# Kernel optimization log

Measured on AMD Instinct MI355X. Metric: run time of the kernel, lower is better.

The kernel has to match this reference:

```python
import jax, jax.numpy as jnp
import numpy as np

H = 4096          # hidden_size
NIN = 17          # RFSIZE*RFSIZE + ADDINPUT + NBACTIONS = 9+4+4
NA = 4            # NBACTIONS


def setup_inputs() -> dict:
    key = jax.random.key(0)
    ks = jax.random.split(key, 12)
    return {
        "x": jax.random.normal(ks[0], (1, NIN), jnp.float32),
        "hidden": 0.1 * jax.random.normal(ks[1], (1, H), jnp.float32),
        "hebb": 0.01 * jax.random.normal(ks[2], (H, H), jnp.float32),
        "i2h_w": 0.1 * jax.random.normal(ks[3], (H, NIN), jnp.float32),
        "i2h_b": 0.1 * jax.random.normal(ks[4], (H,), jnp.float32),
        "w": 0.01 * jax.random.uniform(ks[5], (H, H), jnp.float32),
        "alpha": 0.01 * jax.random.uniform(ks[6], (H, H), jnp.float32),
        "eta": 0.01 * jnp.ones((1,), jnp.float32),
        "h2o_w": 0.1 * jax.random.normal(ks[7], (NA, H), jnp.float32),
        "h2o_b": 0.1 * jax.random.normal(ks[8], (NA,), jnp.float32),
        "h2v_w": 0.1 * jax.random.normal(ks[9], (1, H), jnp.float32),
        "h2v_b": 0.1 * jax.random.normal(ks[10], (1,), jnp.float32),
    }


def reference(x, hidden, hebb, i2h_w, i2h_b, w, alpha, eta, h2o_w, h2o_b, h2v_w, h2v_b):
    # plastic RNN step: h = tanh(i2h(x) + hidden @ (w + alpha*hebb))
    h = jnp.tanh(x @ i2h_w.T + i2h_b + hidden @ (w + alpha * hebb))  # [1,H]
    # Hebbian trace update: (1-eta)*hebb + eta * outer(hidden, h)
    hebb_new = (1.0 - eta) * hebb + eta * (hidden[0][:, None] * h[0][None, :])  # [H,H]
    activout = jax.nn.softmax(h @ h2o_w.T + h2o_b, axis=-1)  # [1,NA]
    valueout = h @ h2v_w.T + h2v_b                           # [1,1]
    return activout, valueout, h, hebb_new
```

## Files before the change

kernel.cpp:

```cpp
#include <hip/hip_runtime.h>

#define HDIM 4096
#define NIN 17
#define NA 4

using f4 = __attribute__((ext_vector_type(4))) float;

constexpr int TB = 256;
constexpr int CPT = 4;
constexpr int BXC = HDIM / (TB * CPT);
constexpr int NCHUNK = 1024;
constexpr int RPC = HDIM / NCHUNK;
constexpr size_t NELEM = (size_t)HDIM * HDIM;

__global__ void k_matvec(const float* __restrict__ w, const float* __restrict__ alpha,
                         const float* __restrict__ hebb, const float* __restrict__ hidden,
                         float* __restrict__ partial, float* __restrict__ acc5) {
    if (blockIdx.x == 0 && blockIdx.y == 0 && threadIdx.x < 8) acc5[threadIdx.x] = 0.f;
    const int col0 = (blockIdx.x * TB + threadIdx.x) * CPT;
    const int row0 = blockIdx.y * RPC;
    const size_t base = (size_t)row0 * HDIM + col0;

    f4 wv[RPC], av[RPC], bv[RPC];
#pragma unroll
    for (int r = 0; r < RPC; ++r) {
        const size_t off = base + (size_t)r * HDIM;
        wv[r] = __builtin_nontemporal_load((const f4*)(w + off));
        av[r] = __builtin_nontemporal_load((const f4*)(alpha + off));
        bv[r] = *(const f4*)(hebb + off);
    }
    f4 acc = {0.f, 0.f, 0.f, 0.f};
#pragma unroll
    for (int r = 0; r < RPC; ++r) {
        const float hv = hidden[row0 + r];
        acc += hv * (wv[r] + av[r] * bv[r]);
    }
    *(f4*)(partial + (size_t)blockIdx.y * HDIM + col0) = acc;
}

constexpr int HC = 32;
constexpr int HGRP = TB / HC;
constexpr int HCPG = NCHUNK / HGRP;

__global__ void k_hact(const float* __restrict__ partial, const float* __restrict__ x,
                       const float* __restrict__ i2h_w, const float* __restrict__ i2h_b,
                       const float* __restrict__ h2o_w, const float* __restrict__ h2v_w,
                       float* __restrict__ h_f, float* __restrict__ h_out,
                       float* __restrict__ acc5) {
    const int tid = threadIdx.x;
    const int lane = tid & (HC - 1);
    const int grp = tid >> 5;
    const int col = blockIdx.x * HC + lane;

    float s = 0.f;
    const float* p = partial + (size_t)(grp * HCPG) * HDIM + col;
#pragma unroll 16
    for (int c = 0; c < HCPG; ++c) s += p[(size_t)c * HDIM];

    __shared__ float red[TB];
    red[tid] = s;
    __syncthreads();
    for (int st = TB / 2; st >= HC; st >>= 1) {
        if (tid < st) red[tid] += red[tid + st];
        __syncthreads();
    }
    if (tid < HC) {
        float z = red[tid] + i2h_b[col];
#pragma unroll
        for (int k = 0; k < NIN; ++k) z += x[k] * i2h_w[col * NIN + k];
        const float h = tanhf(z);
        h_f[col] = h;
        h_out[col] = h;
        float d[NA + 1];
#pragma unroll
        for (int a = 0; a < NA; ++a) d[a] = h * h2o_w[(size_t)a * HDIM + col];
        d[NA] = h * h2v_w[col];
#pragma unroll
        for (int a = 0; a <= NA; ++a) {
            float v = d[a];
#pragma unroll
            for (int sft = 16; sft > 0; sft >>= 1) v += __shfl_down(v, sft, 32);
            if (lane == 0) atomicAdd(acc5 + a, v);
        }
    }
}

__global__ void k_hebb(const float* __restrict__ hebb, const float* __restrict__ hidden,
                       const float* __restrict__ h_f, const float* __restrict__ eta,
                       float* __restrict__ hebb_out) {
    const size_t t = (size_t)blockIdx.x * TB + threadIdx.x;
    const size_t s = 4 * t + 3;
    const float e = eta[0];
    const float om = 1.f - e;

    if (t == 0) {
        const float hv0 = e * hidden[0];
        hebb_out[0] = om * hebb[0] + hv0 * h_f[0];
        hebb_out[1] = om * hebb[1] + hv0 * h_f[1];
        hebb_out[2] = om * hebb[2] + hv0 * h_f[2];
    }

    if (s + 3 < NELEM) {
        const float b0 = hebb[s];
        const f4 bv = *(const f4*)(hebb + s + 1);
        const float b[4] = {b0, bv.x, bv.y, bv.z};
        f4 v;
#pragma unroll
        for (int k = 0; k < 4; ++k) {
            const size_t m = s + (size_t)k;
            const int i = (int)(m >> 12);
            const int jj = (int)(m & (HDIM - 1));
            v[k] = om * b[k] + e * hidden[i] * h_f[jj];
        }
        __builtin_nontemporal_store(v, (f4*)(hebb_out + s));
    } else {
        for (size_t m = s; m < NELEM; ++m) {
            const int i = (int)(m >> 12);
            const int jj = (int)(m & (HDIM - 1));
            hebb_out[m] = om * hebb[m] + e * hidden[i] * h_f[jj];
        }
    }
}

__global__ __launch_bounds__(64)
void k_finish(const float* __restrict__ acc5,
              const float* __restrict__ h2o_b, const float* __restrict__ h2v_b,
              float* __restrict__ out) {
    if (threadIdx.x == 0) {
        float o[NA];
        float mx = -1e30f;
#pragma unroll
        for (int a = 0; a < NA; ++a) { o[a] = acc5[a] + h2o_b[a]; mx = fmaxf(mx, o[a]); }
        float se = 0.f;
#pragma unroll
        for (int a = 0; a < NA; ++a) { o[a] = __expf(o[a] - mx); se += o[a]; }
#pragma unroll
        for (int a = 0; a < NA; ++a) out[a] = o[a] / se;
        out[NA] = acc5[NA] + h2v_b[0];
    }
}

extern "C" void kernel_launch(void* const* d_in, const int* in_sizes, int n_in,
                              void* d_out, int out_size, void* d_ws, size_t ws_size,
                              hipStream_t stream) {
    const float* x      = (const float*)d_in[0];
    const float* hidden = (const float*)d_in[1];
    const float* hebb   = (const float*)d_in[2];
    const float* i2h_w  = (const float*)d_in[3];
    const float* i2h_b  = (const float*)d_in[4];
    const float* w      = (const float*)d_in[5];
    const float* alpha  = (const float*)d_in[6];
    const float* eta    = (const float*)d_in[7];
    const float* h2o_w  = (const float*)d_in[8];
    const float* h2o_b  = (const float*)d_in[9];
    const float* h2v_w  = (const float*)d_in[10];
    const float* h2v_b  = (const float*)d_in[11];
    float* out = (float*)d_out;

    float* h_out    = out + 5;
    float* hebb_out = out + 5 + HDIM;

    float* partial = out + 8192;

    float* h_f  = (float*)d_ws;
    float* acc5 = h_f + HDIM;

    k_matvec<<<dim3(BXC, NCHUNK), TB, 0, stream>>>(w, alpha, hebb, hidden, partial, acc5);
    k_hact<<<HDIM / HC, TB, 0, stream>>>(partial, x, i2h_w, i2h_b, h2o_w, h2v_w, h_f, h_out, acc5);
    k_hebb<<<(int)((NELEM / 4) / TB), TB, 0, stream>>>(hebb, hidden, h_f, eta, hebb_out);
    k_finish<<<1, 64, 0, stream>>>(acc5, h2o_b, h2v_b, out);
}
```

Baseline: 255.7 us.

## Fuse matvec and activation into one kernel with in-block column reduction

```diff
diff --git a/kernel.cpp b/kernel.cpp
--- a/kernel.cpp
+++ b/kernel.cpp
@@ -6,89 +6,80 @@
 
 using f4 = __attribute__((ext_vector_type(4))) float;
 
-constexpr int TB = 256;
-constexpr int CPT = 4;
-constexpr int BXC = HDIM / (TB * CPT);
-constexpr int NCHUNK = 1024;
-constexpr int RPC = HDIM / NCHUNK;
+constexpr int TB1 = 1024;
+constexpr int CPB = 16;
+constexpr int NBLK1 = HDIM / CPB;
+constexpr int RPP = TB1 / 4;
+constexpr int NPASS = HDIM / RPP;
 constexpr size_t NELEM = (size_t)HDIM * HDIM;
 
-__global__ void k_matvec(const float* __restrict__ w, const float* __restrict__ alpha,
-                         const float* __restrict__ hebb, const float* __restrict__ hidden,
-                         float* __restrict__ partial, float* __restrict__ acc5) {
-    if (blockIdx.x == 0 && blockIdx.y == 0 && threadIdx.x < 8) acc5[threadIdx.x] = 0.f;
-    const int col0 = (blockIdx.x * TB + threadIdx.x) * CPT;
-    const int row0 = blockIdx.y * RPC;
-    const size_t base = (size_t)row0 * HDIM + col0;
+__global__ __launch_bounds__(TB1)
+void k_mvh(const float* __restrict__ w, const float* __restrict__ alpha,
+           const float* __restrict__ hebb, const float* __restrict__ hidden,
+           const float* __restrict__ x, const float* __restrict__ i2h_w,
+           const float* __restrict__ i2h_b,
+           const float* __restrict__ h2o_w, const float* __restrict__ h2v_w,
+           float* __restrict__ h_f, float* __restrict__ out,
+           float* __restrict__ acc5) {
+    const int tid = threadIdx.x;
+    const int q = tid & 3;
+    const int rw = tid >> 2;
+    const int colq = blockIdx.x * CPB + q * 4;
 
-    f4 wv[RPC], av[RPC], bv[RPC];
-#pragma unroll
-    for (int r = 0; r < RPC; ++r) {
-        const size_t off = base + (size_t)r * HDIM;
-        wv[r] = __builtin_nontemporal_load((const f4*)(w + off));
-        av[r] = __builtin_nontemporal_load((const f4*)(alpha + off));
-        bv[r] = *(const f4*)(hebb + off);
+    f4 acc = {0.f, 0.f, 0.f, 0.f};
+#pragma unroll 4
+    for (int p = 0; p < NPASS; ++p) {
+        const int r = p * RPP + rw;
+        const size_t off = (size_t)r * HDIM + colq;
+        const f4 wv = *(const f4*)(w + off);
+        const f4 av = *(const f4*)(alpha + off);
+        const f4 bv = *(const f4*)(hebb + off);
+        acc += hidden[r] * (wv + av * bv);
     }
-    f4 acc = {0.f, 0.f, 0.f, 0.f};
-#pragma unroll
-    for (int r = 0; r < RPC; ++r) {
-        const float hv = hidden[row0 + r];
-        acc += hv * (wv[r] + av[r] * bv[r]);
-    }
-    *(f4*)(partial + (size_t)blockIdx.y * HDIM + col0) = acc;
-}
 
-constexpr int HC = 32;
-constexpr int HGRP = TB / HC;
-constexpr int HCPG = NCHUNK / HGRP;
-
-__global__ void k_hact(const float* __restrict__ partial, const float* __restrict__ x,
-                       const float* __restrict__ i2h_w, const float* __restrict__ i2h_b,
-                       const float* __restrict__ h2o_w, const float* __restrict__ h2v_w,
-                       float* __restrict__ h_f, float* __restrict__ h_out,
-                       float* __restrict__ acc5) {
-    const int tid = threadIdx.x;
-    const int lane = tid & (HC - 1);
-    const int grp = tid >> 5;
-    const int col = blockIdx.x * HC + lane;
-
-    float s = 0.f;
-    const float* p = partial + (size_t)(grp * HCPG) * HDIM + col;
-#pragma unroll 16
-    for (int c = 0; c < HCPG; ++c) s += p[(size_t)c * HDIM];
-
-    __shared__ float red[TB];
-    red[tid] = s;
+    __shared__ f4 red[TB1];
+    red[tid] = acc;
     __syncthreads();
-    for (int st = TB / 2; st >= HC; st >>= 1) {
-        if (tid < st) red[tid] += red[tid + st];
+    for (int s = TB1 / 2; s >= 4; s >>= 1) {
+        if (tid < s) red[tid] += red[tid + s];
         __syncthreads();
     }
-    if (tid < HC) {
-        float z = red[tid] + i2h_b[col];
+
+    __shared__ float hsh[CPB];
+    if (tid < CPB) {
+        const int j = blockIdx.x * CPB + tid;
+        float z = red[tid >> 2][tid & 3] + i2h_b[j];
 #pragma unroll
-        for (int k = 0; k < NIN; ++k) z += x[k] * i2h_w[col * NIN + k];
+        for (int k = 0; k < NIN; ++k) z += x[k] * i2h_w[j * NIN + k];
         const float h = tanhf(z);
-        h_f[col] = h;
-        h_out[col] = h;
-        float d[NA + 1];
+        h_f[j] = h;
+        out[5 + j] = h;
+        hsh[tid] = h;
+    }
+    __syncthreads();
+
+    if (tid == 0) {
+        float a5[NA + 1] = {0.f, 0.f, 0.f, 0.f, 0.f};
 #pragma unroll
-        for (int a = 0; a < NA; ++a) d[a] = h * h2o_w[(size_t)a * HDIM + col];
-        d[NA] = h * h2v_w[col];
+        for (int c = 0; c < CPB; ++c) {
+            const int j = blockIdx.x * CPB + c;
+            const float h = hsh[c];
 #pragma unroll
-        for (int a = 0; a <= NA; ++a) {
-            float v = d[a];
+            for (int a = 0; a < NA; ++a) a5[a] += h * h2o_w[(size_t)a * HDIM + j];
+            a5[NA] += h * h2v_w[j];
+        }
 #pragma unroll
-            for (int sft = 16; sft > 0; sft >>= 1) v += __shfl_down(v, sft, 32);
-            if (lane == 0) atomicAdd(acc5 + a, v);
-        }
+        for (int a = 0; a <= NA; ++a) atomicAdd(acc5 + a, a5[a]);
     }
 }
 
-__global__ void k_hebb(const float* __restrict__ hebb, const float* __restrict__ hidden,
-                       const float* __restrict__ h_f, const float* __restrict__ eta,
-                       float* __restrict__ hebb_out) {
-    const size_t t = (size_t)blockIdx.x * TB + threadIdx.x;
+constexpr int TB2 = 256;
+
+__global__ __launch_bounds__(TB2)
+void k_hebb(const float* __restrict__ hebb, const float* __restrict__ hidden,
+            const float* __restrict__ h_f, const float* __restrict__ eta,
+            float* __restrict__ hebb_out) {
+    const size_t t = (size_t)blockIdx.x * TB2 + threadIdx.x;
     const size_t s = 4 * t + 3;
     const float e = eta[0];
     const float om = 1.f - e;
@@ -157,16 +148,14 @@
     const float* h2v_b  = (const float*)d_in[11];
     float* out = (float*)d_out;
 
-    float* h_out    = out + 5;
     float* hebb_out = out + 5 + HDIM;
-
-    float* partial = out + 8192;
 
     float* h_f  = (float*)d_ws;
     float* acc5 = h_f + HDIM;
 
-    k_matvec<<<dim3(BXC, NCHUNK), TB, 0, stream>>>(w, alpha, hebb, hidden, partial, acc5);
-    k_hact<<<HDIM / HC, TB, 0, stream>>>(partial, x, i2h_w, i2h_b, h2o_w, h2v_w, h_f, h_out, acc5);
-    k_hebb<<<(int)((NELEM / 4) / TB), TB, 0, stream>>>(hebb, hidden, h_f, eta, hebb_out);
+    hipMemsetAsync(acc5, 0, 8 * sizeof(float), stream);
+    k_mvh<<<NBLK1, TB1, 0, stream>>>(w, alpha, hebb, hidden, x, i2h_w, i2h_b,
+                                     h2o_w, h2v_w, h_f, out, acc5);
+    k_hebb<<<(int)((NELEM / 4) / TB2), TB2, 0, stream>>>(hebb, hidden, h_f, eta, hebb_out);
     k_finish<<<1, 64, 0, stream>>>(acc5, h2o_b, h2v_b, out);
 }
```

After: 277.7 us. 8.6% more time.

## Fold softmax finish into hact via last-block counter; widen hebb per-thread work

Applied to the files above, without the earlier changes.

```diff
diff --git a/kernel.cpp b/kernel.cpp
--- a/kernel.cpp
+++ b/kernel.cpp
@@ -15,8 +15,12 @@
 
 __global__ void k_matvec(const float* __restrict__ w, const float* __restrict__ alpha,
                          const float* __restrict__ hebb, const float* __restrict__ hidden,
-                         float* __restrict__ partial, float* __restrict__ acc5) {
-    if (blockIdx.x == 0 && blockIdx.y == 0 && threadIdx.x < 8) acc5[threadIdx.x] = 0.f;
+                         float* __restrict__ partial, float* __restrict__ acc5,
+                         unsigned* __restrict__ cnt) {
+    if (blockIdx.x == 0 && blockIdx.y == 0 && threadIdx.x < 9) {
+        if (threadIdx.x < 8) acc5[threadIdx.x] = 0.f;
+        else *cnt = 0u;
+    }
     const int col0 = (blockIdx.x * TB + threadIdx.x) * CPT;
     const int row0 = blockIdx.y * RPC;
     const size_t base = (size_t)row0 * HDIM + col0;
@@ -44,9 +48,11 @@
 
 __global__ void k_hact(const float* __restrict__ partial, const float* __restrict__ x,
                        const float* __restrict__ i2h_w, const float* __restrict__ i2h_b,
-                       const float* __restrict__ h2o_w, const float* __restrict__ h2v_w,
+                       const float* __restrict__ h2o_w, const float* __restrict__ h2o_b,
+                       const float* __restrict__ h2v_w, const float* __restrict__ h2v_b,
                        float* __restrict__ h_f, float* __restrict__ h_out,
-                       float* __restrict__ acc5) {
+                       float* __restrict__ acc5, unsigned* __restrict__ cnt,
+                       float* __restrict__ out) {
     const int tid = threadIdx.x;
     const int lane = tid & (HC - 1);
     const int grp = tid >> 5;
@@ -83,60 +89,79 @@
             if (lane == 0) atomicAdd(acc5 + a, v);
         }
     }
+    if (tid == 0) {
+        __threadfence();
+        if (atomicAdd(cnt, 1u) == (HDIM / HC) - 1) {
+            float res[NA + 1];
+#pragma unroll
+            for (int a = 0; a <= NA; ++a) res[a] = atomicAdd(acc5 + a, 0.f);
+            float o[NA];
+            float mx = -1e30f;
+#pragma unroll
+            for (int a = 0; a < NA; ++a) { o[a] = res[a] + h2o_b[a]; mx = fmaxf(mx, o[a]); }
+            float se = 0.f;
+#pragma unroll
+            for (int a = 0; a < NA; ++a) { o[a] = __expf(o[a] - mx); se += o[a]; }
+#pragma unroll
+            for (int a = 0; a < NA; ++a) out[a] = o[a] / se;
+            out[NA] = res[NA] + h2v_b[0];
+        }
+    }
 }
+
+constexpr size_t NQK = 4194303;
+constexpr int HEB_BLK = 4096;
 
 __global__ void k_hebb(const float* __restrict__ hebb, const float* __restrict__ hidden,
                        const float* __restrict__ h_f, const float* __restrict__ eta,
                        float* __restrict__ hebb_out) {
-    const size_t t = (size_t)blockIdx.x * TB + threadIdx.x;
-    const size_t s = 4 * t + 3;
+    const int tid = threadIdx.x;
+    const size_t gt = (size_t)blockIdx.x * TB + tid;
+    const size_t wid = gt >> 6;
+    const int lane = tid & 63;
     const float e = eta[0];
     const float om = 1.f - e;
 
-    if (t == 0) {
+    if (gt == 0) {
         const float hv0 = e * hidden[0];
         hebb_out[0] = om * hebb[0] + hv0 * h_f[0];
         hebb_out[1] = om * hebb[1] + hv0 * h_f[1];
         hebb_out[2] = om * hebb[2] + hv0 * h_f[2];
+        hebb_out[NELEM - 1] = om * hebb[NELEM - 1] + e * hidden[HDIM - 1] * h_f[HDIM - 1];
     }
 
-    if (s + 3 < NELEM) {
-        const float b0 = hebb[s];
-        const f4 bv = *(const f4*)(hebb + s + 1);
-        const float b[4] = {b0, bv.x, bv.y, bv.z};
-        f4 v;
+    size_t k[4];
+    bool ok[4];
+    float b0[4];
+    f4 bv[4];
 #pragma unroll
-        for (int k = 0; k < 4; ++k) {
-            const size_t m = s + (size_t)k;
-            const int i = (int)(m >> 12);
-            const int jj = (int)(m & (HDIM - 1));
-            v[k] = om * b[k] + e * hidden[i] * h_f[jj];
-        }
-        __builtin_nontemporal_store(v, (f4*)(hebb_out + s));
-    } else {
-        for (size_t m = s; m < NELEM; ++m) {
-            const int i = (int)(m >> 12);
-            const int jj = (int)(m & (HDIM - 1));
-            hebb_out[m] = om * hebb[m] + e * hidden[i] * h_f[jj];
+    for (int q = 0; q < 4; ++q) {
+        k[q] = wid * 256 + (size_t)lane + (size_t)q * 64;
+        ok[q] = k[q] < NQK;
+    }
+#pragma unroll
+    for (int q = 0; q < 4; ++q) {
+        if (ok[q]) {
+            const size_t s = 4 * k[q] + 3;
+            b0[q] = hebb[s];
+            bv[q] = *(const f4*)(hebb + s + 1);
         }
     }
-}
-
-__global__ __launch_bounds__(64)
-void k_finish(const float* __restrict__ acc5,
-              const float* __restrict__ h2o_b, const float* __restrict__ h2v_b,
-              float* __restrict__ out) {
-    if (threadIdx.x == 0) {
-        float o[NA];
-        float mx = -1e30f;
 #pragma unroll
-        for (int a = 0; a < NA; ++a) { o[a] = acc5[a] + h2o_b[a]; mx = fmaxf(mx, o[a]); }
-        float se = 0.f;
+    for (int q = 0; q < 4; ++q) {
+        if (ok[q]) {
+            const size_t s = 4 * k[q] + 3;
+            const float b[4] = {b0[q], bv[q].x, bv[q].y, bv[q].z};
+            f4 v;
 #pragma unroll
-        for (int a = 0; a < NA; ++a) { o[a] = __expf(o[a] - mx); se += o[a]; }
-#pragma unroll
-        for (int a = 0; a < NA; ++a) out[a] = o[a] / se;
-        out[NA] = acc5[NA] + h2v_b[0];
+            for (int kk = 0; kk < 4; ++kk) {
+                const size_t m = s + (size_t)kk;
+                const int i = (int)(m >> 12);
+                const int jj = (int)(m & (HDIM - 1));
+                v[kk] = om * b[kk] + e * hidden[i] * h_f[jj];
+            }
+            __builtin_nontemporal_store(v, (f4*)(hebb_out + s));
+        }
     }
 }
 
@@ -164,9 +189,10 @@
 
     float* h_f  = (float*)d_ws;
     float* acc5 = h_f + HDIM;
+    unsigned* cnt = (unsigned*)(acc5 + 8);
 
-    k_matvec<<<dim3(BXC, NCHUNK), TB, 0, stream>>>(w, alpha, hebb, hidden, partial, acc5);
-    k_hact<<<HDIM / HC, TB, 0, stream>>>(partial, x, i2h_w, i2h_b, h2o_w, h2v_w, h_f, h_out, acc5);
-    k_hebb<<<(int)((NELEM / 4) / TB), TB, 0, stream>>>(hebb, hidden, h_f, eta, hebb_out);
-    k_finish<<<1, 64, 0, stream>>>(acc5, h2o_b, h2v_b, out);
+    k_matvec<<<dim3(BXC, NCHUNK), TB, 0, stream>>>(w, alpha, hebb, hidden, partial, acc5, cnt);
+    k_hact<<<HDIM / HC, TB, 0, stream>>>(partial, x, i2h_w, i2h_b, h2o_w, h2o_b,
+                                         h2v_w, h2v_b, h_f, h_out, acc5, cnt, out);
+    k_hebb<<<HEB_BLK, TB, 0, stream>>>(hebb, hidden, h_f, eta, hebb_out);
 }
```

Measured after the change: 258.8 us. Within noise of the previous version (+1.2%).
